# Performance work log

Measured on AMD Instinct MI355X. Metric: run time of the kernel, lower is better.

Reference implementation:

```python
import jax, jax.numpy as jnp
import numpy as np

B_, T_, DIN, H, DZ, DX = 64, 256, 128, 256, 8, 8


def setup_inputs() -> dict:
    key = jax.random.key(0)
    ks = jax.random.split(key, 13)
    p = lambda k, sh: jax.random.normal(k, sh, dtype=jnp.float32) * 0.05
    return {
        "y": jax.random.normal(ks[0], (B_, T_, DIN), dtype=jnp.float32),
        "W_ih": p(ks[1], (3 * H, DIN)), "W_hh": p(ks[2], (3 * H, H)),
        "b_ih": p(ks[3], (3 * H,)), "b_hh": p(ks[4], (3 * H,)),
        "W_mz": p(ks[5], (DZ, H)), "b_mz": p(ks[6], (DZ,)),
        "W_mx": p(ks[7], (DX, H)), "b_mx": p(ks[8], (DX,)),
        "W_pz": p(ks[9], (2 * DZ, H)), "b_pz": p(ks[10], (2 * DZ,)),
        "W_cx": p(ks[11], (DX * DX, H)), "b_cx": p(ks[12], (DX * DX,)),
    }


def _gru(y, W_ih, W_hh, b_ih, b_hh):
    # torch nn.GRU (single layer, unidirectional, batch_first)
    B, T, _ = y.shape
    Hh = W_hh.shape[1]
    x_proj = jnp.einsum('btd,gd->btg', y, W_ih) + b_ih  # [B,T,3H]

    def step(h, xp):
        hp = h @ W_hh.T + b_hh
        xr, xz, xn = jnp.split(xp, 3, axis=-1)
        hr, hz, hn = jnp.split(hp, 3, axis=-1)
        r = jax.nn.sigmoid(xr + hr)
        z = jax.nn.sigmoid(xz + hz)
        n = jnp.tanh(xn + r * hn)
        h_new = (1.0 - z) * n + z * h
        return h_new, h_new

    h0 = jnp.zeros((B, Hh), dtype=y.dtype)
    _, hs = jax.lax.scan(step, h0, jnp.swapaxes(x_proj, 0, 1))
    return jnp.swapaxes(hs, 0, 1)  # [B,T,H]


def _forward(y, W_ih, W_hh, b_ih, b_hh, W_mz, b_mz, W_mx, b_mx, W_pz, b_pz, W_cx, b_cx):
    enc = _gru(y, W_ih, W_hh, b_ih, b_hh)                       # [B,T,H]
    mean_z = enc @ W_mz.T + b_mz                                 # [B,T,DZ]
    mean_x = enc @ W_mx.T + b_mx                                 # [B,T,DX]
    bd_z = enc @ W_pz.T + b_pz                                   # [B,T,2*DZ]  (apply_softplus=False)

    # banded cov: per latent dim, upper-bidiagonal cholesky factor [B,T,T]
    diag = jnp.moveaxis(jax.nn.softplus(bd_z[..., :DZ]), -1, 0)  # [DZ,B,T]
    off = jnp.moveaxis(bd_z[:, :-1, DZ:], -1, 0)                 # [DZ,B,T-1]
    B, T = diag.shape[1], diag.shape[2]
    idx = jnp.arange(T)
    chol_z = (jnp.zeros((DZ, B, T, T), dtype=y.dtype)
              .at[:, :, idx, idx].set(diag)
              .at[:, :, idx[:-1], idx[1:]].set(off))             # [DZ,B,T,T]

    # anchor first two x-dims at t=0 (in-place mutation in torch)
    mean_x = mean_x.at[:, :, :2].add(-mean_x[:, 0:1, :2])
    mean_x_flat = mean_x.reshape(B * T, DX)

    cov_x = enc @ W_cx.T + b_cx                                  # [B,T,DX*DX]
    cov_x_flat = cov_x.reshape(B * T, DX, DX)
    return mean_z, chol_z, mean_x_flat, cov_x_flat


def reference(y, W_ih, W_hh, b_ih, b_hh, W_mz, b_mz, W_mx, b_mx, W_pz, b_pz, W_cx, b_cx):
    return _forward(y, W_ih, W_hh, b_ih, b_hh, W_mz, b_mz, W_mx, b_mx, W_pz, b_pz, W_cx, b_cx)
```

## Files before the change

kernel.cpp:

```cpp
#include <hip/hip_runtime.h>
#include <cstdint>
#include <cstddef>

#define B_   64
#define T_   256
#define DIN_ 128
#define H_   256
#define G3_  768

typedef _Float16 f16x8 __attribute__((ext_vector_type(8)));
typedef float    f32x4 __attribute__((ext_vector_type(4)));

#define MFMA(a, b, c) __builtin_amdgcn_mfma_f32_16x16x32_f16((a), (b), (c), 0, 0, 0)

__device__ __forceinline__ unsigned short f2h(float f) {
  _Float16 h = (_Float16)f;
  return __builtin_bit_cast(unsigned short, h);
}

__global__ __launch_bounds__(256) void prep_kernel(
    const float* __restrict__ W_ih, const float* __restrict__ W_hh,
    const float* __restrict__ W_mz, const float* __restrict__ W_mx,
    const float* __restrict__ W_pz, const float* __restrict__ W_cx,
    float* __restrict__ WT_ih, float* __restrict__ WheadT,
    unsigned* __restrict__ Wreg) {
  int i = blockIdx.x * 256 + threadIdx.x;
  if (i < 98304) {
    int k = i / 768, g = i % 768;
    WT_ih[i] = W_ih[g * 128 + k];
  } else if (i < 98304 + 24576) {
    int j = i - 98304;
    int c = j >> 8, k = j & 255;
    float v;
    if (c < 8)       v = W_mz[c * 256 + k];
    else if (c < 16) v = W_mx[(c - 8) * 256 + k];
    else if (c < 32) v = W_pz[(c - 16) * 256 + k];
    else             v = W_cx[(c - 32) * 256 + k];
    WheadT[j] = v;
  } else {
    int m = i - 122880;
    int d = m & 3, n = m >> 2;
    int tid = n & 1023, fi = n >> 10;
    int g  = fi >> 3, kf = fi & 7;
    int wv = tid >> 6, l = tid & 63;
    int u = wv * 16 + (l & 15);
    int k = kf * 32 + ((l >> 4) << 3) + 2 * d;
    int row = g * 256 + u;
    unsigned short lo = f2h(W_hh[row * 256 + k]);
    unsigned short hi = f2h(W_hh[row * 256 + k + 1]);
    Wreg[m] = ((unsigned)hi << 16) | (unsigned)lo;
  }
}

__global__ __launch_bounds__(256) void xproj_kernel(
    const float* __restrict__ y, const float* __restrict__ WT_ih,
    const float* __restrict__ b_ih, const float* __restrict__ b_hh,
    float* __restrict__ xp) {
  __shared__ float ylds[64][132];
  int tid = threadIdx.x;
  int row0 = (blockIdx.x >> 1) * 64;
  int c0 = (blockIdx.x & 1) * 3;
  const float4* y4 = (const float4*)(y + (size_t)row0 * DIN_);
#pragma unroll
  for (int i = 0; i < 8; ++i) {
    int idx = i * 256 + tid;
    float4 v = y4[idx];
    int r = idx >> 5, c4 = (idx & 31) * 4;
    ylds[r][c4 + 0] = v.x; ylds[r][c4 + 1] = v.y;
    ylds[r][c4 + 2] = v.z; ylds[r][c4 + 3] = v.w;
  }
  __syncthreads();
  int tx = tid & 15, ty = tid >> 4;
  for (int c = c0; c < c0 + 3; ++c) {
    int col0 = c * 128 + tx * 8;
    float acc[4][8];
#pragma unroll
    for (int a = 0; a < 4; ++a)
#pragma unroll
      for (int b = 0; b < 8; ++b) acc[a][b] = 0.f;
#pragma unroll 4
    for (int k = 0; k < 128; ++k) {
      float4 w0 = *(const float4*)&WT_ih[k * 768 + col0];
      float4 w1 = *(const float4*)&WT_ih[k * 768 + col0 + 4];
      float a0 = ylds[ty * 4 + 0][k], a1 = ylds[ty * 4 + 1][k];
      float a2 = ylds[ty * 4 + 2][k], a3 = ylds[ty * 4 + 3][k];
      acc[0][0] += a0 * w0.x; acc[0][1] += a0 * w0.y; acc[0][2] += a0 * w0.z; acc[0][3] += a0 * w0.w;
      acc[0][4] += a0 * w1.x; acc[0][5] += a0 * w1.y; acc[0][6] += a0 * w1.z; acc[0][7] += a0 * w1.w;
      acc[1][0] += a1 * w0.x; acc[1][1] += a1 * w0.y; acc[1][2] += a1 * w0.z; acc[1][3] += a1 * w0.w;
      acc[1][4] += a1 * w1.x; acc[1][5] += a1 * w1.y; acc[1][6] += a1 * w1.z; acc[1][7] += a1 * w1.w;
      acc[2][0] += a2 * w0.x; acc[2][1] += a2 * w0.y; acc[2][2] += a2 * w0.z; acc[2][3] += a2 * w0.w;
      acc[2][4] += a2 * w1.x; acc[2][5] += a2 * w1.y; acc[2][6] += a2 * w1.z; acc[2][7] += a2 * w1.w;
      acc[3][0] += a3 * w0.x; acc[3][1] += a3 * w0.y; acc[3][2] += a3 * w0.z; acc[3][3] += a3 * w0.w;
      acc[3][4] += a3 * w1.x; acc[3][5] += a3 * w1.y; acc[3][6] += a3 * w1.z; acc[3][7] += a3 * w1.w;
    }
    float4 b0 = *(const float4*)&b_ih[col0];
    float4 b1 = *(const float4*)&b_ih[col0 + 4];
    if (c < 4) {
      float4 h0 = *(const float4*)&b_hh[col0];
      float4 h1 = *(const float4*)&b_hh[col0 + 4];
      b0.x += h0.x; b0.y += h0.y; b0.z += h0.z; b0.w += h0.w;
      b1.x += h1.x; b1.y += h1.y; b1.z += h1.z; b1.w += h1.w;
    }
#pragma unroll
    for (int a = 0; a < 4; ++a) {
      int row = row0 + ty * 4 + a;
      float4 o0, o1;
      o0.x = acc[a][0] + b0.x; o0.y = acc[a][1] + b0.y; o0.z = acc[a][2] + b0.z; o0.w = acc[a][3] + b0.w;
      o1.x = acc[a][4] + b1.x; o1.y = acc[a][5] + b1.y; o1.z = acc[a][6] + b1.z; o1.w = acc[a][7] + b1.w;
      *(float4*)&xp[(size_t)row * G3_ + col0] = o0;
      *(float4*)&xp[(size_t)row * G3_ + col0 + 4] = o1;
    }
  }
}

__global__ __launch_bounds__(1024) void gru_kernel(
    const float* __restrict__ xp, const unsigned* __restrict__ Wreg,
    const float* __restrict__ b_hh, float* enc, float4* __restrict__ cholU) {
  int tid = threadIdx.x;
  int b = blockIdx.x;
  if (b >= 64) {
    float4 zz = {0.f, 0.f, 0.f, 0.f};
    int idx = (b - 64) * 1024 + tid;
    for (; idx < 4194304; idx += 98304) cholU[idx] = zz;
    return;
  }
  int w = tid >> 6;
  int l = tid & 63;
  int g16 = l >> 4;
  int u = w * 16 + (l & 15);
  __shared__ alignas(16) unsigned short h16[2][256];

  f16x8 wfR[8], wfZ[8], wfN[8];
  const uint4* W4 = (const uint4*)Wreg;
#pragma unroll
  for (int kf = 0; kf < 8; ++kf) {
    wfR[kf] = __builtin_bit_cast(f16x8, W4[(0 * 8 + kf) * 1024 + tid]);
    wfZ[kf] = __builtin_bit_cast(f16x8, W4[(1 * 8 + kf) * 1024 + tid]);
    wfN[kf] = __builtin_bit_cast(f16x8, W4[(2 * 8 + kf) * 1024 + tid]);
  }
  if (tid < 32) {
    uint4 z = {0u, 0u, 0u, 0u};
    ((uint4*)h16)[tid] = z;
  }
  const float* xpb = xp + (size_t)b * (T_ * G3_);
  float* encb = enc + (size_t)b * (T_ * H_);
  float bhn = b_hh[512 + u];
  float hold = 0.f;
  const f32x4 z4 = {0.f, 0.f, 0.f, 0.f};
  __syncthreads();
  const uint4* h4 = (const uint4*)h16;
  for (int t = 0; t < T_; ++t) {
    asm volatile("" ::: "memory");
    const float* xq = xpb + (size_t)t * G3_;
    float xr = xq[u], xz = xq[256 + u], xn = xq[512 + u];
    int cur = t & 1;
    f32x4 aR, aZ, aN;
    {
      uint4 hq = h4[cur * 32 + g16];
      f16x8 hk = __builtin_bit_cast(f16x8, hq);
      aR = MFMA(hk, wfR[0], z4);
      aZ = MFMA(hk, wfZ[0], z4);
      aN = MFMA(hk, wfN[0], z4);
    }
#pragma unroll
    for (int kf = 1; kf < 8; ++kf) {
      uint4 hq = h4[cur * 32 + kf * 4 + g16];
      f16x8 hk = __builtin_bit_cast(f16x8, hq);
      aR = MFMA(hk, wfR[kf], aR);
      aZ = MFMA(hk, wfZ[kf], aZ);
      aN = MFMA(hk, wfN[kf], aN);
    }
    float pr = aR[0] + xr, pz = aZ[0] + xz;
    float r_ = 1.f / (1.f + __expf(-pr));
    float q_ = 1.f / (1.f + __expf(-pz));
    float zh = q_ * hold, om = 1.f - q_;
    float pn = aN[0] + bhn;
    float a = xn + r_ * pn;
    a = fminf(15.f, fmaxf(-15.f, a));
    float e = __expf(2.f * a);
    float n = (e - 1.f) / (e + 1.f);
    float hn = om * n + zh;
    hold = hn;
    if (g16 == 0) {
      encb[t * 256 + u] = hn;
      h16[cur ^ 1][u] = f2h(hn);
    }
    __syncthreads();
  }
}

__global__ __launch_bounds__(384) void heads_kernel(
    const float* __restrict__ enc, const float* __restrict__ WheadT,
    const float* __restrict__ b_mz, const float* __restrict__ b_mx,
    const float* __restrict__ b_pz, const float* __restrict__ b_cx,
    float* __restrict__ out_meanz, float* __restrict__ out_meanx,
    float* __restrict__ out_covx, float* __restrict__ stage,
    float* __restrict__ chol, float* __restrict__ anchor,
    const float* __restrict__ W_mx) {
  int tid = threadIdx.x;
  if (blockIdx.x >= 512) {
    __shared__ float red[4];
    int bid = blockIdx.x - 512;
    int b = bid >> 1, d = bid & 1;
    if (tid < 256) {
      float v = enc[(size_t)b * (T_ * H_) + tid] * W_mx[d * 256 + tid];
#pragma unroll
      for (int off = 32; off >= 1; off >>= 1) v += __shfl_down(v, off, 64);
      if ((tid & 63) == 0) red[tid >> 6] = v;
    }
    __syncthreads();
    if (tid == 0)
      anchor[b * 2 + d] = b_mx[d] + ((red[0] + red[1]) + (red[2] + red[3]));
    return;
  }
  __shared__ float el[32 * 256];
  int row0 = blockIdx.x * 32;
  const float4* e4 = (const float4*)(enc + (size_t)row0 * 256);
  float4* el4 = (float4*)el;
#pragma unroll
  for (int i = 0; i < 6; ++i) {
    int idx = i * 384 + tid;
    if (idx < 2048) el4[idx] = e4[idx];
  }
  __syncthreads();
  int rg = tid / 96, c = tid - rg * 96;
  const float4* Wc = (const float4*)(WheadT + c * 256);
  float acc[8];
#pragma unroll
  for (int r = 0; r < 8; ++r) acc[r] = 0.f;
  for (int k4 = 0; k4 < 64; ++k4) {
    float4 w4 = Wc[k4];
#pragma unroll
    for (int r = 0; r < 8; ++r) {
      float4 ev = el4[(rg * 8 + r) * 64 + k4];
      acc[r] += w4.x * ev.x; acc[r] += w4.y * ev.y;
      acc[r] += w4.z * ev.z; acc[r] += w4.w * ev.w;
    }
  }
#pragma unroll
  for (int r = 0; r < 8; ++r) {
    int row = row0 + rg * 8 + r;
    float a_ = acc[r];
    if (c < 8) {
      out_meanz[(size_t)row * 8 + c] = a_ + b_mz[c];
    } else if (c < 16) {
      int d = c - 8;
      out_meanx[(size_t)row * 8 + d] = a_ + b_mx[d];
    } else if (c < 32) {
      int d = c - 16;
      float v = a_ + b_pz[d];
      if (d < 8)
        v = (v > 0.f) ? (v + log1pf(__expf(-v))) : log1pf(__expf(v));
      int bb = row >> 8, tt = row & 255;
      if (d < 4) {
        stage[(size_t)row * 16 + d] = v;
      } else if (d < 8) {
        chol[(((size_t)d * 64 + bb) * 256 + tt) * 256 + tt] = v;
      } else if (d < 12) {
        stage[(size_t)row * 16 + d] = v;
      } else {
        int dd = d - 8;
        if (tt < 255)
          chol[(((size_t)dd * 64 + bb) * 256 + tt) * 256 + tt + 1] = v;
      }
    } else {
      int d = c - 32;
      out_covx[(size_t)row * 64 + d] = a_ + b_cx[d];
    }
  }
}

__global__ __launch_bounds__(256) void chol_fin(
    const float* __restrict__ stage, float4* __restrict__ chol,
    const float* __restrict__ anchor, float* __restrict__ mean_x) {
  int i = blockIdx.x * 256 + threadIdx.x;
  int stride = gridDim.x * 256;
  for (; i < 4227072; i += stride) {
    if (i < 4194304) {
      int d = i >> 20;
      int bt = (i >> 6) & 16383;
      int t = bt & 255;
      int lane = i & 63;
      float vd = 0.f, vo = 0.f;
      if ((t >> 2) == lane)       vd = stage[bt * 16 + d];
      if (((t + 1) >> 2) == lane) vo = stage[bt * 16 + 8 + d];
      int te = t & 3, oe = (t + 1) & 3;
      float4 v;
      v.x = (te == 0 ? vd : 0.f) + (oe == 0 ? vo : 0.f);
      v.y = (te == 1 ? vd : 0.f) + (oe == 1 ? vo : 0.f);
      v.z = (te == 2 ? vd : 0.f) + (oe == 2 ? vo : 0.f);
      v.w = (te == 3 ? vd : 0.f) + (oe == 3 ? vo : 0.f);
      chol[i] = v;
    } else {
      int j2 = i - 4194304;
      int row = j2 >> 1, d = j2 & 1;
      mean_x[(size_t)row * 8 + d] -= anchor[(row >> 8) * 2 + d];
    }
  }
}

extern "C" void kernel_launch(void* const* d_in, const int* in_sizes, int n_in,
                              void* d_out, int out_size, void* d_ws, size_t ws_size,
                              hipStream_t stream) {
  const float* y    = (const float*)d_in[0];
  const float* W_ih = (const float*)d_in[1];
  const float* W_hh = (const float*)d_in[2];
  const float* b_ih = (const float*)d_in[3];
  const float* b_hh = (const float*)d_in[4];
  const float* W_mz = (const float*)d_in[5];
  const float* b_mz = (const float*)d_in[6];
  const float* W_mx = (const float*)d_in[7];
  const float* b_mx = (const float*)d_in[8];
  const float* W_pz = (const float*)d_in[9];
  const float* b_pz = (const float*)d_in[10];
  const float* W_cx = (const float*)d_in[11];
  const float* b_cx = (const float*)d_in[12];

  float* out    = (float*)d_out;
  float* mean_z = out;
  float* chol   = out + 131072;
  float* mean_x = out + 33685504;
  float* cov_x  = out + 33816576;

  float* ws      = (float*)d_ws;
  float* WT_ih   = ws;
  float* WheadT  = ws + 98304;
  unsigned* Wreg = (unsigned*)(ws + 122880);
  float* anchor  = ws + 221184;
  float* stage   = ws + 221312;

  float* xp  = chol;
  float* enc = chol + 12582912;

  prep_kernel<<<864, 256, 0, stream>>>(W_ih, W_hh, W_mz, W_mx, W_pz, W_cx,
                                       WT_ih, WheadT, Wreg);
  xproj_kernel<<<512, 256, 0, stream>>>(y, WT_ih, b_ih, b_hh, xp);
  gru_kernel<<<160, 1024, 0, stream>>>(xp, Wreg, b_hh, enc,
                                       ((float4*)chol) + 4194304);
  heads_kernel<<<640, 384, 0, stream>>>(enc, WheadT, b_mz, b_mx, b_pz, b_cx,
                                        mean_z, mean_x, cov_x, stage,
                                        chol, anchor, W_mx);
  chol_fin<<<4096, 256, 0, stream>>>(stage, (float4*)chol, anchor, mean_x);
}
```

Measured before the change: 546.0 us.

## Replace MFMA recurrent matvec with v_dot2 dot products and shuffle reduction

The GRU recurrence switches from MFMA 16x16x32 instructions, where only column 0 of the output was used, to per-lane v_dot2_f32_f16 dot products. Each of the four lane quads covers a 64-wide slice of K, and the partial sums are combined with xor shuffles. The W_hh register layout in the prep kernel is reordered to match. The x-projection loads for the next step are also prefetched one step ahead. This avoids MFMA latency and wasted output lanes on the serial critical path. The cost is 96 more scalar dot instructions per step plus the shuffles.

```diff
diff --git a/kernel.cpp b/kernel.cpp
--- a/kernel.cpp
+++ b/kernel.cpp
@@ -8,14 +8,13 @@
 #define H_   256
 #define G3_  768
 
-typedef _Float16 f16x8 __attribute__((ext_vector_type(8)));
-typedef float    f32x4 __attribute__((ext_vector_type(4)));
-
-#define MFMA(a, b, c) __builtin_amdgcn_mfma_f32_16x16x32_f16((a), (b), (c), 0, 0, 0)
-
 __device__ __forceinline__ unsigned short f2h(float f) {
   _Float16 h = (_Float16)f;
   return __builtin_bit_cast(unsigned short, h);
+}
+
+__device__ __forceinline__ void dot2f(float& acc, unsigned a, unsigned b) {
+  asm("v_dot2_f32_f16 %0, %1, %2, %0" : "+v"(acc) : "v"(a), "v"(b));
 }
 
 __global__ __launch_bounds__(256) void prep_kernel(
@@ -39,12 +38,14 @@
     WheadT[j] = v;
   } else {
     int m = i - 122880;
-    int d = m & 3, n = m >> 2;
-    int tid = n & 1023, fi = n >> 10;
-    int g  = fi >> 3, kf = fi & 7;
+    int j = m & 3, n = m >> 2;
+    int tid = n & 1023, c = n >> 10;
+    int fi = 4 * c + j;
+    int g = fi >> 5, p = fi & 31;
     int wv = tid >> 6, l = tid & 63;
     int u = wv * 16 + (l & 15);
-    int k = kf * 32 + ((l >> 4) << 3) + 2 * d;
+    int q = l >> 4;
+    int k = q * 64 + 2 * p;
     int row = g * 256 + u;
     unsigned short lo = f2h(W_hh[row * 256 + k]);
     unsigned short hi = f2h(W_hh[row * 256 + k + 1]);
@@ -126,65 +127,70 @@
   }
   int w = tid >> 6;
   int l = tid & 63;
-  int g16 = l >> 4;
+  int q = l >> 4;
   int u = w * 16 + (l & 15);
   __shared__ alignas(16) unsigned short h16[2][256];
 
-  f16x8 wfR[8], wfZ[8], wfN[8];
+  unsigned wg[96];
   const uint4* W4 = (const uint4*)Wreg;
 #pragma unroll
-  for (int kf = 0; kf < 8; ++kf) {
-    wfR[kf] = __builtin_bit_cast(f16x8, W4[(0 * 8 + kf) * 1024 + tid]);
-    wfZ[kf] = __builtin_bit_cast(f16x8, W4[(1 * 8 + kf) * 1024 + tid]);
-    wfN[kf] = __builtin_bit_cast(f16x8, W4[(2 * 8 + kf) * 1024 + tid]);
+  for (int c = 0; c < 24; ++c) {
+    uint4 qd = W4[c * 1024 + tid];
+    wg[4 * c + 0] = qd.x; wg[4 * c + 1] = qd.y;
+    wg[4 * c + 2] = qd.z; wg[4 * c + 3] = qd.w;
   }
   if (tid < 32) {
     uint4 z = {0u, 0u, 0u, 0u};
     ((uint4*)h16)[tid] = z;
   }
   const float* xpb = xp + (size_t)b * (T_ * G3_);
-  float* encb = enc + (size_t)b * (T_ * H_);
+  float* ep = enc + (size_t)b * (T_ * H_) + u;
   float bhn = b_hh[512 + u];
   float hold = 0.f;
-  const f32x4 z4 = {0.f, 0.f, 0.f, 0.f};
+  float xr = xpb[u], xz = xpb[256 + u], xn = xpb[512 + u];
+  const float* xq = xpb + G3_;
   __syncthreads();
-  const uint4* h4 = (const uint4*)h16;
   for (int t = 0; t < T_; ++t) {
     asm volatile("" ::: "memory");
-    const float* xq = xpb + (size_t)t * G3_;
-    float xr = xq[u], xz = xq[256 + u], xn = xq[512 + u];
+    float nxr = xq[u], nxz = xq[256 + u], nxn = xq[512 + u];
+    xq += G3_;
     int cur = t & 1;
-    f32x4 aR, aZ, aN;
-    {
-      uint4 hq = h4[cur * 32 + g16];
-      f16x8 hk = __builtin_bit_cast(f16x8, hq);
-      aR = MFMA(hk, wfR[0], z4);
-      aZ = MFMA(hk, wfZ[0], z4);
-      aN = MFMA(hk, wfN[0], z4);
-    }
-#pragma unroll
-    for (int kf = 1; kf < 8; ++kf) {
-      uint4 hq = h4[cur * 32 + kf * 4 + g16];
-      f16x8 hk = __builtin_bit_cast(f16x8, hq);
-      aR = MFMA(hk, wfR[kf], aR);
-      aZ = MFMA(hk, wfZ[kf], aZ);
-      aN = MFMA(hk, wfN[kf], aN);
-    }
-    float pr = aR[0] + xr, pz = aZ[0] + xz;
-    float r_ = 1.f / (1.f + __expf(-pr));
-    float q_ = 1.f / (1.f + __expf(-pz));
+    const uint4* hb = (const uint4*)&h16[cur][q * 64];
+    float ar = 0.f, az = 0.f, an = 0.f;
+#pragma unroll
+    for (int r8 = 0; r8 < 8; ++r8) {
+      uint4 hq = hb[r8];
+      dot2f(ar, hq.x, wg[(r8 << 2) + 0]);
+      dot2f(ar, hq.y, wg[(r8 << 2) + 1]);
+      dot2f(ar, hq.z, wg[(r8 << 2) + 2]);
+      dot2f(ar, hq.w, wg[(r8 << 2) + 3]);
+      dot2f(az, hq.x, wg[32 + (r8 << 2) + 0]);
+      dot2f(az, hq.y, wg[32 + (r8 << 2) + 1]);
+      dot2f(az, hq.z, wg[32 + (r8 << 2) + 2]);
+      dot2f(az, hq.w, wg[32 + (r8 << 2) + 3]);
+      dot2f(an, hq.x, wg[64 + (r8 << 2) + 0]);
+      dot2f(an, hq.y, wg[64 + (r8 << 2) + 1]);
+      dot2f(an, hq.z, wg[64 + (r8 << 2) + 2]);
+      dot2f(an, hq.w, wg[64 + (r8 << 2) + 3]);
+    }
+    ar += __shfl_xor(ar, 16, 64);  ar += __shfl_xor(ar, 32, 64);
+    az += __shfl_xor(az, 16, 64);  az += __shfl_xor(az, 32, 64);
+    an += __shfl_xor(an, 16, 64);  an += __shfl_xor(an, 32, 64);
+    float r_ = 1.f / (1.f + __expf(-(ar + xr)));
+    float q_ = 1.f / (1.f + __expf(-(az + xz)));
     float zh = q_ * hold, om = 1.f - q_;
-    float pn = aN[0] + bhn;
-    float a = xn + r_ * pn;
+    float a = xn + r_ * (an + bhn);
     a = fminf(15.f, fmaxf(-15.f, a));
     float e = __expf(2.f * a);
     float n = (e - 1.f) / (e + 1.f);
     float hn = om * n + zh;
     hold = hn;
-    if (g16 == 0) {
-      encb[t * 256 + u] = hn;
+    if (q == 0) {
+      *ep = hn;
       h16[cur ^ 1][u] = f2h(hn);
     }
+    ep += 256;
+    xr = nxr; xz = nxz; xn = nxn;
     __syncthreads();
   }
 }
```

After: 681.8 us. +24.9%, slower.
